# Optimization experiments

Measured on AMD Instinct MI355X. Metric: run time of the kernel, lower is better.

The kernel has to match this reference:

```python
import jax, jax.numpy as jnp
import numpy as np


def setup_inputs() -> dict:
    key = jax.random.key(0)
    ks = jax.random.split(key, 7)
    S, A, I, H = 2000, 1000, 5, 32
    return {
        "g": jax.random.normal(ks[0], (S, A, I), dtype=jnp.float32),
        "W1": jax.random.normal(ks[1], (A, I, H), dtype=jnp.float32) * (1.0 / np.sqrt(I)),
        "b1": jax.random.normal(ks[2], (A, H), dtype=jnp.float32) * 0.01,
        "W2": jax.random.normal(ks[3], (A, H, H), dtype=jnp.float32) * (1.0 / np.sqrt(H)),
        "b2": jax.random.normal(ks[4], (A, H), dtype=jnp.float32) * 0.01,
        "W3": jax.random.normal(ks[5], (A, H, 1), dtype=jnp.float32) * (1.0 / np.sqrt(H)),
        "b3": jax.random.normal(ks[6], (A, 1), dtype=jnp.float32) * 0.01,
    }


def reference(g, W1, b1, W2, b2, W3, b3):
    # Batched equivalent of the nested per-struct / per-atom Python loop:
    # each atom `a` has its own tiny MLP (5 -> 32 -> 32 -> 1, tanh),
    # applied to g[s, a] for every structure s. Grouped-GEMM form:
    # s = struct, a = atom, i/h/o = feature dims.
    h1 = jnp.tanh(jnp.einsum('sai,aih->sah', g, W1) + b1[None, :, :])
    h2 = jnp.tanh(jnp.einsum('sah,aho->sao', h1, W2) + b2[None, :, :])
    e = jnp.einsum('sah,aho->sao', h2, W3) + b3[None, :, :]
    # e_nn has shape [n_struct, n_atoms], matching the torch buffer.
    return e[..., 0]
```

## Files before the change

### kernel.cpp

```cpp
#include <hip/hip_runtime.h>
#include <hip/hip_bf16.h>

#define NS_TOT 2000
#define NA 1000
#define NI 5
#define NH 32
#define SHALF 1000
#define W2LD 40

typedef __attribute__((ext_vector_type(2)))  float f32x2;
typedef __attribute__((ext_vector_type(8)))  short short8;
typedef __attribute__((ext_vector_type(16))) float f32x16;

struct f4pair  { f32x2 a, b; };
struct accpair { f32x2 p[8]; };

__device__ __forceinline__ f32x2 tanh_pk(f32x2 X) {
    f32x2 z = X * X;
    f32x2 n = (z + 105.0f) * z + 945.0f;
    f32x2 d = (z * 15.0f + 420.0f) * z + 945.0f;
    const float rr = __builtin_amdgcn_rcpf(d.x * d.y);
    f32x2 r;
    r.x = rr * d.y;
    r.y = rr * d.x;
    f32x2 t = X * n * r;
    t.x = __builtin_amdgcn_fmed3f(t.x, -1.0f, 1.0f);
    t.y = __builtin_amdgcn_fmed3f(t.y, -1.0f, 1.0f);
    return t;
}

__device__ __forceinline__ unsigned short f2bf_rne(float x) {
    unsigned u = __float_as_uint(x);
    unsigned r = u + 0x7FFFu + ((u >> 16) & 1u);
    return (unsigned short)(r >> 16);
}
__device__ __forceinline__ unsigned pack2(float a, float b) {
    __hip_bfloat162 p = __float22bfloat162_rn(make_float2(a, b));
    unsigned u; __builtin_memcpy(&u, &p, 4); return u;
}
__device__ __forceinline__ unsigned tanh2_pack(float a, float b) {
    f32x2 X = {a, b};
    f32x2 t = tanh_pk(X);
    return pack2(t.x, t.y);
}

__global__ __attribute__((amdgpu_flat_work_group_size(256, 256),
                          amdgpu_waves_per_eu(3, 4)))
void mlp_mfma(
    const float* __restrict__ g,
    const float* __restrict__ W1, const float* __restrict__ b1,
    const float* __restrict__ W2, const float* __restrict__ b2,
    const float* __restrict__ W3, const float* __restrict__ b3,
    float* __restrict__ out)
{
    const int bid   = blockIdx.x;
    const int araw  = bid % NA;
    const int chunk = bid / NA;
    const int a = (araw >> 3) + 125 * (araw & 7);
    const int t = threadIdx.x;
    const int lane = t & 63, wid = t >> 6;
    const int l31 = lane & 31, half = lane >> 5;

    const int sbase_blk = chunk * SHALF;
    const int send      = sbase_blk + SHALF;

    __shared__ __align__(16) unsigned short sW2T[NH * W2LD];
    __shared__ __align__(16) unsigned short sW1T[NH * 8];
    __shared__ __align__(16) float sB2[NH];
    __shared__ __align__(16) float sW3[NH];

    for (int idx = t; idx < NH * NH; idx += 256) {
        const int i = idx >> 5, j = idx & 31;
        sW2T[j * W2LD + i] = f2bf_rne(W2[(size_t)a * NH * NH + idx]);
    }
    if (t < NH) {
        sB2[t] = b2[a * NH + t];
        sW3[t] = W3[a * NH + t];
        const int m = t;
        #pragma unroll
        for (int i = 0; i < NI; ++i)
            sW1T[m * 8 + i] = f2bf_rne(W1[(size_t)a * NI * NH + i * NH + m]);
        sW1T[m * 8 + 5] = f2bf_rne(b1[a * NH + m]);
        sW1T[m * 8 + 6] = 0;
        sW1T[m * 8 + 7] = 0;
    }
    __syncthreads();

    const short8 zero8 = {0,0,0,0,0,0,0,0};
    const short8 w1ld = __builtin_bit_cast(short8, *(const uint4*)(sW1T + l31 * 8));
    const short8 afl1 = half ? zero8 : w1ld;
    const short8 af0 = __builtin_bit_cast(short8, *(const uint4*)(sW2T + l31 * W2LD + half * 8));
    const short8 af1 = __builtin_bit_cast(short8, *(const uint4*)(sW2T + l31 * W2LD + 16 + half * 8));
    const float4 b2q0 = ((const float4*)sB2)[0 + half];
    const float4 b2q1 = ((const float4*)sB2)[2 + half];
    const float4 b2q2 = ((const float4*)sB2)[4 + half];
    const float4 b2q3 = ((const float4*)sB2)[6 + half];
    const float4 w3q0 = ((const float4*)sW3)[0 + half];
    const float4 w3q1 = ((const float4*)sW3)[2 + half];
    const float4 w3q2 = ((const float4*)sW3)[4 + half];
    const float4 w3q3 = ((const float4*)sW3)[6 + half];
    const float bias3 = b3[a];
    const f4pair w3p0 = __builtin_bit_cast(f4pair, w3q0);
    const f4pair w3p1 = __builtin_bit_cast(f4pair, w3q1);
    const f4pair w3p2 = __builtin_bit_cast(f4pair, w3q2);
    const f4pair w3p3 = __builtin_bit_cast(f4pair, w3q3);
    const f32x16 zacc = {0,0,0,0,0,0,0,0,0,0,0,0,0,0,0,0};
    const f32x16 b2acc = {b2q0.x, b2q0.y, b2q0.z, b2q0.w,
                          b2q1.x, b2q1.y, b2q1.z, b2q1.w,
                          b2q2.x, b2q2.y, b2q2.z, b2q2.w,
                          b2q3.x, b2q3.y, b2q3.z, b2q3.w};

    #define BUILD_L1(AX0, AX1, AX2, AX3, AX4) { \
        const unsigned gp01 = pack2(AX0, AX1); \
        const unsigned gp23 = pack2(AX2, AX3); \
        const unsigned gp45 = pack2(AX4, 1.0f); \
        auto gs01 = __builtin_amdgcn_permlane32_swap(gp01, gp01, false, false); \
        auto gs23 = __builtin_amdgcn_permlane32_swap(gp23, gp23, false, false); \
        auto gs45 = __builtin_amdgcn_permlane32_swap(gp45, gp45, false, false); \
        const uint4 bu0 = make_uint4(gp01,    gp23,    gp45,    0u); \
        const uint4 bu1 = make_uint4(gs01[1], gs23[1], gs45[1], 0u); \
        const short8 gb0 = __builtin_bit_cast(short8, bu0); \
        const short8 gb1 = __builtin_bit_cast(short8, bu1); \
        d0 = __builtin_amdgcn_mfma_f32_32x32x16_bf16(afl1, gb0, zacc, 0, 0, 0); \
        d1 = __builtin_amdgcn_mfma_f32_32x32x16_bf16(afl1, gb1, zacc, 0, 0, 0); }

    float x0g, x1g, x2g, x3g, x4g;
    float y0g, y1g, y2g, y3g, y4g;
    {
        const int s0 = sbase_blk + wid * 64 + lane;
        const float* gp = g + ((size_t)s0 * NA + a) * NI;
        x0g = gp[0]; x1g = gp[1]; x2g = gp[2]; x3g = gp[3]; x4g = gp[4];
        const int s1 = s0 + 256;
        const float* gq = g + ((size_t)s1 * NA + a) * NI;
        y0g = gq[0]; y1g = gq[1]; y2g = gq[2]; y3g = gq[3]; y4g = gq[4];
    }
    f32x16 d0, d1;
    BUILD_L1(x0g, x1g, x2g, x3g, x4g)

    #pragma unroll
    for (int it = 0; it < 4; ++it) {
        const int base = sbase_blk + it * 256 + wid * 64;
        const int s = base + lane;

        short8 bk0_0, bk1_0, bk0_1, bk1_1;
        #define TILE_CONV(DD, BK0, BK1) { \
            const unsigned p0 = tanh2_pack(DD[0],  DD[1]); \
            const unsigned p1 = tanh2_pack(DD[2],  DD[3]); \
            const unsigned p2 = tanh2_pack(DD[4],  DD[5]); \
            const unsigned p3 = tanh2_pack(DD[6],  DD[7]); \
            const unsigned p4 = tanh2_pack(DD[8],  DD[9]); \
            const unsigned p5 = tanh2_pack(DD[10], DD[11]); \
            const unsigned p6 = tanh2_pack(DD[12], DD[13]); \
            const unsigned p7 = tanh2_pack(DD[14], DD[15]); \
            auto s02 = __builtin_amdgcn_permlane32_swap(p0, p2, false, false); \
            auto s13 = __builtin_amdgcn_permlane32_swap(p1, p3, false, false); \
            auto s46 = __builtin_amdgcn_permlane32_swap(p4, p6, false, false); \
            auto s57 = __builtin_amdgcn_permlane32_swap(p5, p7, false, false); \
            const uint4 u0 = make_uint4(s02[0], s13[0], s02[1], s13[1]); \
            const uint4 u1 = make_uint4(s46[0], s57[0], s46[1], s57[1]); \
            BK0 = __builtin_bit_cast(short8, u0); \
            BK1 = __builtin_bit_cast(short8, u1); }
        TILE_CONV(d0, bk0_0, bk1_0)
        TILE_CONV(d1, bk0_1, bk1_1)
        #undef TILE_CONV

        __builtin_amdgcn_sched_barrier(0);
        if (it < 3) {
            BUILD_L1(y0g, y1g, y2g, y3g, y4g)
        }
        __builtin_amdgcn_sched_barrier(0);

        f32x16 acc0 = __builtin_amdgcn_mfma_f32_32x32x16_bf16(af0, bk0_0, b2acc, 0, 0, 0);
        acc0 = __builtin_amdgcn_mfma_f32_32x32x16_bf16(af1, bk1_0, acc0, 0, 0, 0);
        f32x16 acc1 = __builtin_amdgcn_mfma_f32_32x32x16_bf16(af0, bk0_1, b2acc, 0, 0, 0);
        acc1 = __builtin_amdgcn_mfma_f32_32x32x16_bf16(af1, bk1_1, acc1, 0, 0, 0);

        if (it < 2) {
            const int sn = s + 512;
            const int sln = (sn < send) ? sn : (send - 1);
            const float* gq = g + ((size_t)sln * NA + a) * NI;
            y0g = gq[0]; y1g = gq[1]; y2g = gq[2]; y3g = gq[3]; y4g = gq[4];
        }

        const accpair ap0 = __builtin_bit_cast(accpair, acc0);
        f32x2 p0 = {0.f, 0.f};
        p0 += tanh_pk(ap0.p[0]) * w3p0.a;  p0 += tanh_pk(ap0.p[1]) * w3p0.b;
        p0 += tanh_pk(ap0.p[2]) * w3p1.a;  p0 += tanh_pk(ap0.p[3]) * w3p1.b;
        p0 += tanh_pk(ap0.p[4]) * w3p2.a;  p0 += tanh_pk(ap0.p[5]) * w3p2.b;
        p0 += tanh_pk(ap0.p[6]) * w3p3.a;  p0 += tanh_pk(ap0.p[7]) * w3p3.b;
        const float e0 = p0.x + p0.y;
        const accpair ap1 = __builtin_bit_cast(accpair, acc1);
        f32x2 p1 = {0.f, 0.f};
        p1 += tanh_pk(ap1.p[0]) * w3p0.a;  p1 += tanh_pk(ap1.p[1]) * w3p0.b;
        p1 += tanh_pk(ap1.p[2]) * w3p1.a;  p1 += tanh_pk(ap1.p[3]) * w3p1.b;
        p1 += tanh_pk(ap1.p[4]) * w3p2.a;  p1 += tanh_pk(ap1.p[5]) * w3p2.b;
        p1 += tanh_pk(ap1.p[6]) * w3p3.a;  p1 += tanh_pk(ap1.p[7]) * w3p3.b;
        const float e1 = p1.x + p1.y;
        auto es = __builtin_amdgcn_permlane32_swap(__float_as_uint(e0),
                                                   __float_as_uint(e1),
                                                   false, false);
        const float etot = __uint_as_float(es[0]) + __uint_as_float(es[1]);
        if (s < send) out[(size_t)s * NA + a] = etot + bias3;
    }
    #undef BUILD_L1
}

extern "C" void kernel_launch(void* const* d_in, const int* in_sizes, int n_in,
                              void* d_out, int out_size, void* d_ws, size_t ws_size,
                              hipStream_t stream) {
    const float* g  = (const float*)d_in[0];
    const float* W1 = (const float*)d_in[1];
    const float* b1 = (const float*)d_in[2];
    const float* W2 = (const float*)d_in[3];
    const float* b2 = (const float*)d_in[4];
    const float* W3 = (const float*)d_in[5];
    const float* b3 = (const float*)d_in[6];
    float* out = (float*)d_out;
    mlp_mfma<<<dim3(NA * 2), dim3(256), 0, stream>>>(g, W1, b1, W2, b2, W3, b3, out);
}
```

Measured before the change: 119.7 us.

## Process two 64-struct tiles per wave per iteration, halving loop trips

The loop now runs two iterations per wave instead of four, and each iteration handles two 64-struct groups (A and B). That gives four independent layer-1 MFMAs, four tanh conversions and four layer-2 accumulator chains per iteration, replacing the previous cross-iteration software pipelining that used sched_barriers. The next iteration's g values are prefetched at the start of the first iteration. The waves_per_eu minimum is lowered from 3 to 2 so the compiler can use more registers for the doubled live state. The aim is more instruction-level parallelism with fewer loop boundaries, at the cost of higher register pressure and possibly lower occupancy.

Result: no change. 120.7 us (+0.9%).

```diff
diff --git a/kernel.cpp b/kernel.cpp
--- a/kernel.cpp
+++ b/kernel.cpp
@@ -45,7 +45,7 @@
 }
 
 __global__ __attribute__((amdgpu_flat_work_group_size(256, 256),
-                          amdgpu_waves_per_eu(3, 4)))
+                          amdgpu_waves_per_eu(2, 4)))
 void mlp_mfma(
     const float* __restrict__ g,
     const float* __restrict__ W1, const float* __restrict__ b1,
@@ -95,54 +95,66 @@
     const float4 b2q1 = ((const float4*)sB2)[2 + half];
     const float4 b2q2 = ((const float4*)sB2)[4 + half];
     const float4 b2q3 = ((const float4*)sB2)[6 + half];
-    const float4 w3q0 = ((const float4*)sW3)[0 + half];
-    const float4 w3q1 = ((const float4*)sW3)[2 + half];
-    const float4 w3q2 = ((const float4*)sW3)[4 + half];
-    const float4 w3q3 = ((const float4*)sW3)[6 + half];
+    const f4pair w3p0 = __builtin_bit_cast(f4pair, ((const float4*)sW3)[0 + half]);
+    const f4pair w3p1 = __builtin_bit_cast(f4pair, ((const float4*)sW3)[2 + half]);
+    const f4pair w3p2 = __builtin_bit_cast(f4pair, ((const float4*)sW3)[4 + half]);
+    const f4pair w3p3 = __builtin_bit_cast(f4pair, ((const float4*)sW3)[6 + half]);
     const float bias3 = b3[a];
-    const f4pair w3p0 = __builtin_bit_cast(f4pair, w3q0);
-    const f4pair w3p1 = __builtin_bit_cast(f4pair, w3q1);
-    const f4pair w3p2 = __builtin_bit_cast(f4pair, w3q2);
-    const f4pair w3p3 = __builtin_bit_cast(f4pair, w3q3);
     const f32x16 zacc = {0,0,0,0,0,0,0,0,0,0,0,0,0,0,0,0};
     const f32x16 b2acc = {b2q0.x, b2q0.y, b2q0.z, b2q0.w,
                           b2q1.x, b2q1.y, b2q1.z, b2q1.w,
                           b2q2.x, b2q2.y, b2q2.z, b2q2.w,
                           b2q3.x, b2q3.y, b2q3.z, b2q3.w};
 
-    #define BUILD_L1(AX0, AX1, AX2, AX3, AX4) { \
-        const unsigned gp01 = pack2(AX0, AX1); \
-        const unsigned gp23 = pack2(AX2, AX3); \
-        const unsigned gp45 = pack2(AX4, 1.0f); \
-        auto gs01 = __builtin_amdgcn_permlane32_swap(gp01, gp01, false, false); \
-        auto gs23 = __builtin_amdgcn_permlane32_swap(gp23, gp23, false, false); \
-        auto gs45 = __builtin_amdgcn_permlane32_swap(gp45, gp45, false, false); \
-        const uint4 bu0 = make_uint4(gp01,    gp23,    gp45,    0u); \
-        const uint4 bu1 = make_uint4(gs01[1], gs23[1], gs45[1], 0u); \
-        const short8 gb0 = __builtin_bit_cast(short8, bu0); \
-        const short8 gb1 = __builtin_bit_cast(short8, bu1); \
-        d0 = __builtin_amdgcn_mfma_f32_32x32x16_bf16(afl1, gb0, zacc, 0, 0, 0); \
-        d1 = __builtin_amdgcn_mfma_f32_32x32x16_bf16(afl1, gb1, zacc, 0, 0, 0); }
-
-    float x0g, x1g, x2g, x3g, x4g;
-    float y0g, y1g, y2g, y3g, y4g;
+    float xA0, xA1, xA2, xA3, xA4, xB0, xB1, xB2, xB3, xB4;
     {
-        const int s0 = sbase_blk + wid * 64 + lane;
-        const float* gp = g + ((size_t)s0 * NA + a) * NI;
-        x0g = gp[0]; x1g = gp[1]; x2g = gp[2]; x3g = gp[3]; x4g = gp[4];
-        const int s1 = s0 + 256;
-        const float* gq = g + ((size_t)s1 * NA + a) * NI;
-        y0g = gq[0]; y1g = gq[1]; y2g = gq[2]; y3g = gq[3]; y4g = gq[4];
-    }
-    f32x16 d0, d1;
-    BUILD_L1(x0g, x1g, x2g, x3g, x4g)
+        const int sA = sbase_blk + wid * 128 + lane;
+        const float* gp = g + ((size_t)sA * NA + a) * NI;
+        xA0 = gp[0]; xA1 = gp[1]; xA2 = gp[2]; xA3 = gp[3]; xA4 = gp[4];
+        const float* gq = g + ((size_t)(sA + 64) * NA + a) * NI;
+        xB0 = gq[0]; xB1 = gq[1]; xB2 = gq[2]; xB3 = gq[3]; xB4 = gq[4];
+    }
 
     #pragma unroll
-    for (int it = 0; it < 4; ++it) {
-        const int base = sbase_blk + it * 256 + wid * 64;
-        const int s = base + lane;
-
-        short8 bk0_0, bk1_0, bk0_1, bk1_1;
+    for (int it = 0; it < 2; ++it) {
+        const int sA = sbase_blk + it * 512 + wid * 128 + lane;
+        const int sB = sA + 64;
+
+        float yA0, yA1, yA2, yA3, yA4, yB0, yB1, yB2, yB3, yB4;
+        if (it == 0) {
+            const int pA = sA + 512;
+            const int pAl = (pA < send) ? pA : (send - 1);
+            const float* gp = g + ((size_t)pAl * NA + a) * NI;
+            yA0 = gp[0]; yA1 = gp[1]; yA2 = gp[2]; yA3 = gp[3]; yA4 = gp[4];
+            const int pB = pA + 64;
+            const int pBl = (pB < send) ? pB : (send - 1);
+            const float* gq = g + ((size_t)pBl * NA + a) * NI;
+            yB0 = gq[0]; yB1 = gq[1]; yB2 = gq[2]; yB3 = gq[3]; yB4 = gq[4];
+        }
+
+        const unsigned gA01 = pack2(xA0, xA1);
+        const unsigned gA23 = pack2(xA2, xA3);
+        const unsigned gA45 = pack2(xA4, 1.0f);
+        const unsigned gB01 = pack2(xB0, xB1);
+        const unsigned gB23 = pack2(xB2, xB3);
+        const unsigned gB45 = pack2(xB4, 1.0f);
+        auto hA01 = __builtin_amdgcn_permlane32_swap(gA01, gA01, false, false);
+        auto hA23 = __builtin_amdgcn_permlane32_swap(gA23, gA23, false, false);
+        auto hA45 = __builtin_amdgcn_permlane32_swap(gA45, gA45, false, false);
+        auto hB01 = __builtin_amdgcn_permlane32_swap(gB01, gB01, false, false);
+        auto hB23 = __builtin_amdgcn_permlane32_swap(gB23, gB23, false, false);
+        auto hB45 = __builtin_amdgcn_permlane32_swap(gB45, gB45, false, false);
+        const short8 gb0 = __builtin_bit_cast(short8, make_uint4(gA01, gA23, gA45, 0u));
+        const short8 gb1 = __builtin_bit_cast(short8, make_uint4(hA01[1], hA23[1], hA45[1], 0u));
+        const short8 gb2 = __builtin_bit_cast(short8, make_uint4(gB01, gB23, gB45, 0u));
+        const short8 gb3 = __builtin_bit_cast(short8, make_uint4(hB01[1], hB23[1], hB45[1], 0u));
+
+        f32x16 d0 = __builtin_amdgcn_mfma_f32_32x32x16_bf16(afl1, gb0, zacc, 0, 0, 0);
+        f32x16 d1 = __builtin_amdgcn_mfma_f32_32x32x16_bf16(afl1, gb1, zacc, 0, 0, 0);
+        f32x16 d2 = __builtin_amdgcn_mfma_f32_32x32x16_bf16(afl1, gb2, zacc, 0, 0, 0);
+        f32x16 d3 = __builtin_amdgcn_mfma_f32_32x32x16_bf16(afl1, gb3, zacc, 0, 0, 0);
+
+        short8 bk0_0, bk1_0, bk0_1, bk1_1, bk0_2, bk1_2, bk0_3, bk1_3;
         #define TILE_CONV(DD, BK0, BK1) { \
             const unsigned p0 = tanh2_pack(DD[0],  DD[1]); \
             const unsigned p1 = tanh2_pack(DD[2],  DD[3]); \
@@ -156,53 +168,50 @@
             auto s13 = __builtin_amdgcn_permlane32_swap(p1, p3, false, false); \
             auto s46 = __builtin_amdgcn_permlane32_swap(p4, p6, false, false); \
             auto s57 = __builtin_amdgcn_permlane32_swap(p5, p7, false, false); \
-            const uint4 u0 = make_uint4(s02[0], s13[0], s02[1], s13[1]); \
-            const uint4 u1 = make_uint4(s46[0], s57[0], s46[1], s57[1]); \
-            BK0 = __builtin_bit_cast(short8, u0); \
-            BK1 = __builtin_bit_cast(short8, u1); }
+            BK0 = __builtin_bit_cast(short8, make_uint4(s02[0], s13[0], s02[1], s13[1])); \
+            BK1 = __builtin_bit_cast(short8, make_uint4(s46[0], s57[0], s46[1], s57[1])); }
         TILE_CONV(d0, bk0_0, bk1_0)
         TILE_CONV(d1, bk0_1, bk1_1)
+        TILE_CONV(d2, bk0_2, bk1_2)
+        TILE_CONV(d3, bk0_3, bk1_3)
         #undef TILE_CONV
-
-        __builtin_amdgcn_sched_barrier(0);
-        if (it < 3) {
-            BUILD_L1(y0g, y1g, y2g, y3g, y4g)
-        }
-        __builtin_amdgcn_sched_barrier(0);
 
         f32x16 acc0 = __builtin_amdgcn_mfma_f32_32x32x16_bf16(af0, bk0_0, b2acc, 0, 0, 0);
         acc0 = __builtin_amdgcn_mfma_f32_32x32x16_bf16(af1, bk1_0, acc0, 0, 0, 0);
         f32x16 acc1 = __builtin_amdgcn_mfma_f32_32x32x16_bf16(af0, bk0_1, b2acc, 0, 0, 0);
         acc1 = __builtin_amdgcn_mfma_f32_32x32x16_bf16(af1, bk1_1, acc1, 0, 0, 0);
-
-        if (it < 2) {
-            const int sn = s + 512;
-            const int sln = (sn < send) ? sn : (send - 1);
-            const float* gq = g + ((size_t)sln * NA + a) * NI;
-            y0g = gq[0]; y1g = gq[1]; y2g = gq[2]; y3g = gq[3]; y4g = gq[4];
+        f32x16 acc2 = __builtin_amdgcn_mfma_f32_32x32x16_bf16(af0, bk0_2, b2acc, 0, 0, 0);
+        acc2 = __builtin_amdgcn_mfma_f32_32x32x16_bf16(af1, bk1_2, acc2, 0, 0, 0);
+        f32x16 acc3 = __builtin_amdgcn_mfma_f32_32x32x16_bf16(af0, bk0_3, b2acc, 0, 0, 0);
+        acc3 = __builtin_amdgcn_mfma_f32_32x32x16_bf16(af1, bk1_3, acc3, 0, 0, 0);
+
+        #define EPI(ACC, EOUT) { \
+            const accpair ap = __builtin_bit_cast(accpair, ACC); \
+            f32x2 p = {0.f, 0.f}; \
+            p += tanh_pk(ap.p[0]) * w3p0.a;  p += tanh_pk(ap.p[1]) * w3p0.b; \
+            p += tanh_pk(ap.p[2]) * w3p1.a;  p += tanh_pk(ap.p[3]) * w3p1.b; \
+            p += tanh_pk(ap.p[4]) * w3p2.a;  p += tanh_pk(ap.p[5]) * w3p2.b; \
+            p += tanh_pk(ap.p[6]) * w3p3.a;  p += tanh_pk(ap.p[7]) * w3p3.b; \
+            EOUT = p.x + p.y; }
+        float e0, e1, e2, e3;
+        EPI(acc0, e0) EPI(acc1, e1) EPI(acc2, e2) EPI(acc3, e3)
+        #undef EPI
+        auto es01 = __builtin_amdgcn_permlane32_swap(__float_as_uint(e0),
+                                                     __float_as_uint(e1),
+                                                     false, false);
+        const float et01 = __uint_as_float(es01[0]) + __uint_as_float(es01[1]);
+        if (sA < send) out[(size_t)sA * NA + a] = et01 + bias3;
+        auto es23 = __builtin_amdgcn_permlane32_swap(__float_as_uint(e2),
+                                                     __float_as_uint(e3),
+                                                     false, false);
+        const float et23 = __uint_as_float(es23[0]) + __uint_as_float(es23[1]);
+        if (sB < send) out[(size_t)sB * NA + a] = et23 + bias3;
+
+        if (it == 0) {
+            xA0 = yA0; xA1 = yA1; xA2 = yA2; xA3 = yA3; xA4 = yA4;
+            xB0 = yB0; xB1 = yB1; xB2 = yB2; xB3 = yB3; xB4 = yB4;
         }
-
-        const accpair ap0 = __builtin_bit_cast(accpair, acc0);
-        f32x2 p0 = {0.f, 0.f};
-        p0 += tanh_pk(ap0.p[0]) * w3p0.a;  p0 += tanh_pk(ap0.p[1]) * w3p0.b;
-        p0 += tanh_pk(ap0.p[2]) * w3p1.a;  p0 += tanh_pk(ap0.p[3]) * w3p1.b;
-        p0 += tanh_pk(ap0.p[4]) * w3p2.a;  p0 += tanh_pk(ap0.p[5]) * w3p2.b;
-        p0 += tanh_pk(ap0.p[6]) * w3p3.a;  p0 += tanh_pk(ap0.p[7]) * w3p3.b;
-        const float e0 = p0.x + p0.y;
-        const accpair ap1 = __builtin_bit_cast(accpair, acc1);
-        f32x2 p1 = {0.f, 0.f};
-        p1 += tanh_pk(ap1.p[0]) * w3p0.a;  p1 += tanh_pk(ap1.p[1]) * w3p0.b;
-        p1 += tanh_pk(ap1.p[2]) * w3p1.a;  p1 += tanh_pk(ap1.p[3]) * w3p1.b;
-        p1 += tanh_pk(ap1.p[4]) * w3p2.a;  p1 += tanh_pk(ap1.p[5]) * w3p2.b;
-        p1 += tanh_pk(ap1.p[6]) * w3p3.a;  p1 += tanh_pk(ap1.p[7]) * w3p3.b;
-        const float e1 = p1.x + p1.y;
-        auto es = __builtin_amdgcn_permlane32_swap(__float_as_uint(e0),
-                                                   __float_as_uint(e1),
-                                                   false, false);
-        const float etot = __uint_as_float(es[0]) + __uint_as_float(es[1]);
-        if (s < send) out[(size_t)s * NA + a] = etot + bias3;
-    }
-    #undef BUILD_L1
+    }
 }
 
 extern "C" void kernel_launch(void* const* d_in, const int* in_sizes, int n_in,
```

## Use one 512-thread block per atom and drop layer-1 software pipelining

Applied to the files above, without the earlier changes.

Each block now covers all 2000 structures of one atom with 512 threads, replacing two 256-thread blocks per atom. This halves the per-block W2/W1 shared-memory setup and global weight reads. The layer-1 MFMA is no longer issued a tile ahead behind sched_barriers; it is computed at the top of each iteration, and the g prefetch moves to a register rotation two tiles ahead. Occupancy hints change to waves_per_eu(4,8). The cost is fewer blocks (1000) and less explicit overlap between the layer-1 MFMA and the tanh conversion.

New measurement: 123.8 us. 3.4% more time.

```diff
diff --git a/kernel.cpp b/kernel.cpp
--- a/kernel.cpp
+++ b/kernel.cpp
@@ -5,7 +5,6 @@
 #define NA 1000
 #define NI 5
 #define NH 32
-#define SHALF 1000
 #define W2LD 40
 
 typedef __attribute__((ext_vector_type(2)))  float f32x2;
@@ -44,8 +43,8 @@
     return pack2(t.x, t.y);
 }
 
-__global__ __attribute__((amdgpu_flat_work_group_size(256, 256),
-                          amdgpu_waves_per_eu(3, 4)))
+__global__ __attribute__((amdgpu_flat_work_group_size(512, 512),
+                          amdgpu_waves_per_eu(4, 8)))
 void mlp_mfma(
     const float* __restrict__ g,
     const float* __restrict__ W1, const float* __restrict__ b1,
@@ -53,23 +52,18 @@
     const float* __restrict__ W3, const float* __restrict__ b3,
     float* __restrict__ out)
 {
-    const int bid   = blockIdx.x;
-    const int araw  = bid % NA;
-    const int chunk = bid / NA;
-    const int a = (araw >> 3) + 125 * (araw & 7);
+    const int bid = blockIdx.x;
+    const int a = (bid >> 3) + 125 * (bid & 7);
     const int t = threadIdx.x;
     const int lane = t & 63, wid = t >> 6;
     const int l31 = lane & 31, half = lane >> 5;
-
-    const int sbase_blk = chunk * SHALF;
-    const int send      = sbase_blk + SHALF;
 
     __shared__ __align__(16) unsigned short sW2T[NH * W2LD];
     __shared__ __align__(16) unsigned short sW1T[NH * 8];
     __shared__ __align__(16) float sB2[NH];
     __shared__ __align__(16) float sW3[NH];
 
-    for (int idx = t; idx < NH * NH; idx += 256) {
+    for (int idx = t; idx < NH * NH; idx += 512) {
         const int i = idx >> 5, j = idx & 31;
         sW2T[j * W2LD + i] = f2bf_rne(W2[(size_t)a * NH * NH + idx]);
     }
@@ -95,52 +89,51 @@
     const float4 b2q1 = ((const float4*)sB2)[2 + half];
     const float4 b2q2 = ((const float4*)sB2)[4 + half];
     const float4 b2q3 = ((const float4*)sB2)[6 + half];
-    const float4 w3q0 = ((const float4*)sW3)[0 + half];
-    const float4 w3q1 = ((const float4*)sW3)[2 + half];
-    const float4 w3q2 = ((const float4*)sW3)[4 + half];
-    const float4 w3q3 = ((const float4*)sW3)[6 + half];
+    const f4pair w3p0 = __builtin_bit_cast(f4pair, ((const float4*)sW3)[0 + half]);
+    const f4pair w3p1 = __builtin_bit_cast(f4pair, ((const float4*)sW3)[2 + half]);
+    const f4pair w3p2 = __builtin_bit_cast(f4pair, ((const float4*)sW3)[4 + half]);
+    const f4pair w3p3 = __builtin_bit_cast(f4pair, ((const float4*)sW3)[6 + half]);
     const float bias3 = b3[a];
-    const f4pair w3p0 = __builtin_bit_cast(f4pair, w3q0);
-    const f4pair w3p1 = __builtin_bit_cast(f4pair, w3q1);
-    const f4pair w3p2 = __builtin_bit_cast(f4pair, w3q2);
-    const f4pair w3p3 = __builtin_bit_cast(f4pair, w3q3);
     const f32x16 zacc = {0,0,0,0,0,0,0,0,0,0,0,0,0,0,0,0};
     const f32x16 b2acc = {b2q0.x, b2q0.y, b2q0.z, b2q0.w,
                           b2q1.x, b2q1.y, b2q1.z, b2q1.w,
                           b2q2.x, b2q2.y, b2q2.z, b2q2.w,
                           b2q3.x, b2q3.y, b2q3.z, b2q3.w};
 
-    #define BUILD_L1(AX0, AX1, AX2, AX3, AX4) { \
-        const unsigned gp01 = pack2(AX0, AX1); \
-        const unsigned gp23 = pack2(AX2, AX3); \
-        const unsigned gp45 = pack2(AX4, 1.0f); \
-        auto gs01 = __builtin_amdgcn_permlane32_swap(gp01, gp01, false, false); \
-        auto gs23 = __builtin_amdgcn_permlane32_swap(gp23, gp23, false, false); \
-        auto gs45 = __builtin_amdgcn_permlane32_swap(gp45, gp45, false, false); \
-        const uint4 bu0 = make_uint4(gp01,    gp23,    gp45,    0u); \
-        const uint4 bu1 = make_uint4(gs01[1], gs23[1], gs45[1], 0u); \
-        const short8 gb0 = __builtin_bit_cast(short8, bu0); \
-        const short8 gb1 = __builtin_bit_cast(short8, bu1); \
-        d0 = __builtin_amdgcn_mfma_f32_32x32x16_bf16(afl1, gb0, zacc, 0, 0, 0); \
-        d1 = __builtin_amdgcn_mfma_f32_32x32x16_bf16(afl1, gb1, zacc, 0, 0, 0); }
-
     float x0g, x1g, x2g, x3g, x4g;
     float y0g, y1g, y2g, y3g, y4g;
     {
-        const int s0 = sbase_blk + wid * 64 + lane;
+        const int s0 = wid * 64 + lane;
         const float* gp = g + ((size_t)s0 * NA + a) * NI;
         x0g = gp[0]; x1g = gp[1]; x2g = gp[2]; x3g = gp[3]; x4g = gp[4];
-        const int s1 = s0 + 256;
+        const int s1 = s0 + 512;
         const float* gq = g + ((size_t)s1 * NA + a) * NI;
         y0g = gq[0]; y1g = gq[1]; y2g = gq[2]; y3g = gq[3]; y4g = gq[4];
     }
-    f32x16 d0, d1;
-    BUILD_L1(x0g, x1g, x2g, x3g, x4g)
 
     #pragma unroll
     for (int it = 0; it < 4; ++it) {
-        const int base = sbase_blk + it * 256 + wid * 64;
-        const int s = base + lane;
+        const int s = it * 512 + wid * 64 + lane;
+
+        float n0, n1, n2, n3, n4;
+        if (it < 2) {
+            const int sn = s + 1024;
+            const int sln = (sn < NS_TOT) ? sn : (NS_TOT - 1);
+            const float* gq = g + ((size_t)sln * NA + a) * NI;
+            n0 = gq[0]; n1 = gq[1]; n2 = gq[2]; n3 = gq[3]; n4 = gq[4];
+        }
+
+        const unsigned gp01 = pack2(x0g, x1g);
+        const unsigned gp23 = pack2(x2g, x3g);
+        const unsigned gp45 = pack2(x4g, 1.0f);
+        auto gs01 = __builtin_amdgcn_permlane32_swap(gp01, gp01, false, false);
+        auto gs23 = __builtin_amdgcn_permlane32_swap(gp23, gp23, false, false);
+        auto gs45 = __builtin_amdgcn_permlane32_swap(gp45, gp45, false, false);
+        const short8 gb0 = __builtin_bit_cast(short8, make_uint4(gp01, gp23, gp45, 0u));
+        const short8 gb1 = __builtin_bit_cast(short8, make_uint4(gs01[1], gs23[1], gs45[1], 0u));
+
+        f32x16 d0 = __builtin_amdgcn_mfma_f32_32x32x16_bf16(afl1, gb0, zacc, 0, 0, 0);
+        f32x16 d1 = __builtin_amdgcn_mfma_f32_32x32x16_bf16(afl1, gb1, zacc, 0, 0, 0);
 
         short8 bk0_0, bk1_0, bk0_1, bk1_1;
         #define TILE_CONV(DD, BK0, BK1) { \
@@ -156,31 +149,16 @@
             auto s13 = __builtin_amdgcn_permlane32_swap(p1, p3, false, false); \
             auto s46 = __builtin_amdgcn_permlane32_swap(p4, p6, false, false); \
             auto s57 = __builtin_amdgcn_permlane32_swap(p5, p7, false, false); \
-            const uint4 u0 = make_uint4(s02[0], s13[0], s02[1], s13[1]); \
-            const uint4 u1 = make_uint4(s46[0], s57[0], s46[1], s57[1]); \
-            BK0 = __builtin_bit_cast(short8, u0); \
-            BK1 = __builtin_bit_cast(short8, u1); }
+            BK0 = __builtin_bit_cast(short8, make_uint4(s02[0], s13[0], s02[1], s13[1])); \
+            BK1 = __builtin_bit_cast(short8, make_uint4(s46[0], s57[0], s46[1], s57[1])); }
         TILE_CONV(d0, bk0_0, bk1_0)
         TILE_CONV(d1, bk0_1, bk1_1)
         #undef TILE_CONV
-
-        __builtin_amdgcn_sched_barrier(0);
-        if (it < 3) {
-            BUILD_L1(y0g, y1g, y2g, y3g, y4g)
-        }
-        __builtin_amdgcn_sched_barrier(0);
 
         f32x16 acc0 = __builtin_amdgcn_mfma_f32_32x32x16_bf16(af0, bk0_0, b2acc, 0, 0, 0);
         acc0 = __builtin_amdgcn_mfma_f32_32x32x16_bf16(af1, bk1_0, acc0, 0, 0, 0);
         f32x16 acc1 = __builtin_amdgcn_mfma_f32_32x32x16_bf16(af0, bk0_1, b2acc, 0, 0, 0);
         acc1 = __builtin_amdgcn_mfma_f32_32x32x16_bf16(af1, bk1_1, acc1, 0, 0, 0);
-
-        if (it < 2) {
-            const int sn = s + 512;
-            const int sln = (sn < send) ? sn : (send - 1);
-            const float* gq = g + ((size_t)sln * NA + a) * NI;
-            y0g = gq[0]; y1g = gq[1]; y2g = gq[2]; y3g = gq[3]; y4g = gq[4];
-        }
 
         const accpair ap0 = __builtin_bit_cast(accpair, acc0);
         f32x2 p0 = {0.f, 0.f};
@@ -200,9 +178,11 @@
                                                    __float_as_uint(e1),
                                                    false, false);
         const float etot = __uint_as_float(es[0]) + __uint_as_float(es[1]);
-        if (s < send) out[(size_t)s * NA + a] = etot + bias3;
-    }
-    #undef BUILD_L1
+        if (s < NS_TOT) out[(size_t)s * NA + a] = etot + bias3;
+
+        if (it < 3) { x0g = y0g; x1g = y1g; x2g = y2g; x3g = y3g; x4g = y4g; }
+        if (it < 2) { y0g = n0; y1g = n1; y2g = n2; y3g = n3; y4g = n4; }
+    }
 }
 
 extern "C" void kernel_launch(void* const* d_in, const int* in_sizes, int n_in,
@@ -216,5 +196,5 @@
     const float* W3 = (const float*)d_in[5];
     const float* b3 = (const float*)d_in[6];
     float* out = (float*)d_out;
-    mlp_mfma<<<dim3(NA * 2), dim3(256), 0, stream>>>(g, W1, b1, W2, b2, W3, b3, out);
-}
+    mlp_mfma<<<dim3(NA), dim3(512), 0, stream>>>(g, W1, b1, W2, b2, W3, b3, out);
+}
```
